# Performance work log

Hardware: AMD Instinct MI355X
Metric: run time of the kernel (lower is better)

Reference implementation:

```python
import jax, jax.numpy as jnp
import numpy as np

C_IN = 128
C_INNER = 128


def setup_inputs() -> dict:
    key = jax.random.key(0)
    ks = jax.random.split(key, 9)
    b, c, h, w = 4, C_IN, 64, 64
    s = 1.0 / np.sqrt(c)
    x = jax.random.normal(ks[0], (b, c, h, w), dtype=jnp.float32)
    Wq = jax.random.normal(ks[1], (C_INNER, C_IN), dtype=jnp.float32) * s
    bq = jnp.zeros((C_INNER,), dtype=jnp.float32)
    Wk = jax.random.normal(ks[2], (C_INNER, C_IN), dtype=jnp.float32) * s
    bk = jnp.zeros((C_INNER,), dtype=jnp.float32)
    Wv = jax.random.normal(ks[3], (C_INNER, C_IN), dtype=jnp.float32) * s
    bv = jnp.zeros((C_INNER,), dtype=jnp.float32)
    Wo = jax.random.normal(ks[4], (C_IN, C_INNER), dtype=jnp.float32) * (1.0 / np.sqrt(C_INNER))
    bo = jnp.zeros((C_IN,), dtype=jnp.float32)
    return {"x": x, "Wq": Wq, "bq": bq, "Wk": Wk, "bk": bk,
            "Wv": Wv, "bv": bv, "Wo": Wo, "bo": bo}


def _conv1x1(x, W, bias):
    # x: (b,c,h,w), W: (o,c) -> (b,o,h,w)
    return jnp.einsum('oc,bchw->bohw', W, x) + bias[None, :, None, None]


def reference(x, Wq, bq, Wk, bk, Wv, bv, Wo, bo):
    b, c, h, w = x.shape
    ci = Wq.shape[0]
    n = h * w
    q = _conv1x1(x, Wq, bq).reshape(b, ci, n)          # (b, ci, n)
    k = _conv1x1(x, Wk, bk).reshape(b, ci, n)          # (b, ci, n)
    v = _conv1x1(x, Wv, bv).reshape(b, ci, n)          # (b, ci, n)
    # attn = softmax(q^T @ k) over keys
    attn = jnp.einsum('bci,bcj->bij', q, k)            # (b, n, n)
    attn = jax.nn.softmax(attn, axis=-1)
    out = jnp.einsum('bij,bcj->bci', attn, v)          # (b, ci, n)
    out = out.reshape(b, ci, h, w)
    out = _conv1x1(out, Wo, bo)
    return out + x
```

## Files before the change

### kernel.cpp

```cpp
#include <hip/hip_runtime.h>
#include <math.h>
#include <stdint.h>

#define CDIM 128
#define NTOT 4096
#define LOG2E 1.44269504f

typedef _Float16 f16x8 __attribute__((ext_vector_type(8)));
typedef float floatx4 __attribute__((ext_vector_type(4)));

static __device__ __forceinline__ floatx4 mfma16(f16x8 a, f16x8 b, floatx4 c) {
    return __builtin_amdgcn_mfma_f32_16x16x32_f16(a, b, c, 0, 0, 0);
}
static __device__ __forceinline__ unsigned short f2h(float f) {
    _Float16 h = (_Float16)f;
    return __builtin_bit_cast(unsigned short, h);
}
static __device__ __forceinline__ float h2f(unsigned short u) {
    return (float)__builtin_bit_cast(_Float16, u);
}
static __device__ __forceinline__ float fexp2(float x) {
#if __has_builtin(__builtin_amdgcn_exp2f)
    return __builtin_amdgcn_exp2f(x);
#else
    return exp2f(x);
#endif
}

#define SWZ(row, cc) ((((row) << 7)) + ((((cc) ^ ((row) & 15))) << 3))
#define SWZ8(row, cc) ((((row) << 6)) + ((((cc) ^ ((row) & 7))) << 3))

static __device__ __forceinline__ void gload_lds16(const void* g, void* l) {
    __builtin_amdgcn_global_load_lds(
        (const __attribute__((address_space(1))) void*)g,
        (__attribute__((address_space(3))) void*)l, 16, 0, 0);
}

__global__ __launch_bounds__(256) void qkv_proj_kernel(
    const float* __restrict__ x,
    const float* __restrict__ Wq, const float* __restrict__ Wk,
    const float* __restrict__ Wv,
    const float* __restrict__ bq, const float* __restrict__ bk,
    const float* __restrict__ bv,
    unsigned short* __restrict__ qo, unsigned short* __restrict__ ko,
    unsigned short* __restrict__ vo)
{
    __shared__ __align__(16) unsigned short Xs[64][136];
    __shared__ __align__(16) unsigned short Ws[3][64][136];

    const int t = threadIdx.x, b = blockIdx.y, n0 = blockIdx.x * 64;
    const int zo = blockIdx.z * 64;
    const int w = t >> 6, quad = (t >> 4) & 3, l15 = t & 15;

    {
        const int n = (t & 15) * 4;
        const int c = (t >> 4) * 8;
        float4 xr[8];
        #pragma unroll
        for (int j = 0; j < 8; ++j)
            xr[j] = *(const float4*)&x[((size_t)b * CDIM + c + j) * NTOT + n0 + n];
        #pragma unroll
        for (int k = 0; k < 4; ++k) {
            ushort4 ulo, uhi;
            ulo.x = f2h(((const float*)&xr[0])[k]);
            ulo.y = f2h(((const float*)&xr[1])[k]);
            ulo.z = f2h(((const float*)&xr[2])[k]);
            ulo.w = f2h(((const float*)&xr[3])[k]);
            uhi.x = f2h(((const float*)&xr[4])[k]);
            uhi.y = f2h(((const float*)&xr[5])[k]);
            uhi.z = f2h(((const float*)&xr[6])[k]);
            uhi.w = f2h(((const float*)&xr[7])[k]);
            *(ushort4*)&Xs[n + k][c]     = ulo;
            *(ushort4*)&Xs[n + k][c + 4] = uhi;
        }
    }
    {
        const int o = t >> 2, ch = (t & 3) * 32;
        #pragma unroll
        for (int s = 0; s < 3; ++s) {
            const float* W = (s == 0) ? Wq : (s == 1) ? Wk : Wv;
            #pragma unroll
            for (int i = 0; i < 8; ++i) {
                float4 f4 = *(const float4*)&W[(size_t)(zo + o) * CDIM + ch + i * 4];
                ushort4 u = { f2h(f4.x), f2h(f4.y), f2h(f4.z), f2h(f4.w) };
                *(ushort4*)&Ws[s][o][ch + i * 4] = u;
            }
        }
    }
    __syncthreads();

    f16x8 xf[4];
    #pragma unroll
    for (int f = 0; f < 4; ++f)
        xf[f] = *(const f16x8*)&Xs[w * 16 + l15][f * 32 + quad * 8];

    #pragma unroll
    for (int s = 0; s < 2; ++s) {
        const float* bias = s ? bk : bq;
        unsigned short* dst = s ? ko : qo;
        const float sc = (s == 0) ? LOG2E : 1.0f;
        #pragma unroll
        for (int ot = 0; ot < 4; ++ot) {
            floatx4 acc = (floatx4){0.f, 0.f, 0.f, 0.f};
            #pragma unroll
            for (int f = 0; f < 4; ++f) {
                f16x8 aW = *(const f16x8*)&Ws[s][ot * 16 + l15][f * 32 + quad * 8];
                acc = mfma16(aW, xf[f], acc);
            }
            const int ob = zo + ot * 16 + quad * 4;
            ushort4 u;
            u.x = f2h((acc[0] + bias[ob + 0]) * sc);
            u.y = f2h((acc[1] + bias[ob + 1]) * sc);
            u.z = f2h((acc[2] + bias[ob + 2]) * sc);
            u.w = f2h((acc[3] + bias[ob + 3]) * sc);
            *(ushort4*)&dst[((size_t)b * NTOT + n0 + w * 16 + l15) * CDIM + ob] = u;
        }
    }
    #pragma unroll
    for (int ot = 0; ot < 4; ++ot) {
        floatx4 acc = (floatx4){0.f, 0.f, 0.f, 0.f};
        #pragma unroll
        for (int f = 0; f < 4; ++f) {
            f16x8 bW = *(const f16x8*)&Ws[2][ot * 16 + l15][f * 32 + quad * 8];
            acc = mfma16(xf[f], bW, acc);
        }
        const int o = zo + ot * 16 + l15;
        const float bv_ = bv[o];
        ushort4 u;
        u.x = f2h(acc[0] + bv_); u.y = f2h(acc[1] + bv_);
        u.z = f2h(acc[2] + bv_); u.w = f2h(acc[3] + bv_);
        *(ushort4*)&vo[((size_t)b * CDIM + o) * NTOT + n0 + w * 16 + quad * 4] = u;
    }
}

__global__ __launch_bounds__(512) void attn_kernel(
    const unsigned short* __restrict__ qg,
    const unsigned short* __restrict__ kg,
    const unsigned short* __restrict__ vg,
    unsigned short* __restrict__ Op,
    float* __restrict__ Ms, float* __restrict__ Ls)
{
    __shared__ __align__(16) unsigned short Kb[2][64 * 128];
    __shared__ __align__(16) unsigned short Vb[3][128 * 64];
    __shared__ __align__(16) unsigned short Ps[256 * 64];

    const int t = threadIdx.x;
    const int w = t >> 6, quad = (t >> 4) & 3, l15 = t & 15;

    const int bid = blockIdx.x;
    const int swz = ((bid & 7) << 5) | (bid >> 3);
    const int gidx = swz >> 4;
    const int b = gidx & 3;
    const int z = gidx >> 2;
    const int i0 = (swz & 15) * 256;
    const int jbase = z * 1024;
    const size_t vbase = (size_t)b * CDIM * NTOT;

    f16x8 bQ[2][4];
    #pragma unroll
    for (int nt = 0; nt < 2; ++nt) {
        const size_t qrow = ((size_t)b * NTOT + i0 + w * 32 + nt * 16 + l15) * CDIM;
        #pragma unroll
        for (int f = 0; f < 4; ++f)
            bQ[nt][f] = *(const f16x8*)&qg[qrow + f * 32 + quad * 8];
    }

    auto stageK = [&](unsigned short* Kd, int j0) {
        const size_t kbase = ((size_t)b * NTOT + j0) * CDIM;
        #pragma unroll
        for (int r = 0; r < 2; ++r) {
            const int flat = r * 512 + t;
            const int ldsoff = (r * 512 + (t & ~63)) * 8;
            const int krow = flat >> 4, kcc = flat & 15;
            gload_lds16(&kg[kbase + (size_t)krow * CDIM + ((kcc ^ (krow & 15)) << 3)],
                        &Kd[ldsoff]);
        }
    };
    auto stageV = [&](unsigned short* Vd, int j0) {
        const size_t vrow0 = vbase + j0;
        #pragma unroll
        for (int r = 0; r < 2; ++r) {
            const int flat = r * 512 + t;
            const int ldsoff = (r * 512 + (t & ~63)) * 8;
            const int vrow = flat >> 3, vcc = flat & 7;
            gload_lds16(&vg[vrow0 + (size_t)vrow * NTOT + ((vcc ^ (vrow & 7)) << 3)],
                        &Vd[ldsoff]);
        }
    };

    floatx4 accO[2][8];
    #pragma unroll
    for (int nt = 0; nt < 2; ++nt)
        #pragma unroll
        for (int dt = 0; dt < 8; ++dt) accO[nt][dt] = (floatx4){0.f, 0.f, 0.f, 0.f};
    float m_run[2] = {-INFINITY, -INFINITY};
    float l_part[2] = {0.f, 0.f};

    floatx4 accT[2][4];
    uint2 pu[2][4];
    f16x8 bP[2][2];

    auto QK = [&](const unsigned short* Kd) {
        #pragma unroll
        for (int nt = 0; nt < 2; ++nt)
            #pragma unroll
            for (int jt = 0; jt < 4; ++jt) accT[nt][jt] = (floatx4){0.f, 0.f, 0.f, 0.f};
        __builtin_amdgcn_s_setprio(1);
        #pragma unroll
        for (int jt = 0; jt < 4; ++jt)
            #pragma unroll
            for (int f = 0; f < 4; ++f) {
                f16x8 aK = *(const f16x8*)&Kd[SWZ(jt * 16 + l15, f * 4 + quad)];
                accT[0][jt] = mfma16(aK, bQ[0][f], accT[0][jt]);
                accT[1][jt] = mfma16(aK, bQ[1][f], accT[1][jt]);
            }
        __builtin_amdgcn_s_setprio(0);
    };
    auto RB = [&]() {
        #pragma unroll
        for (int nt = 0; nt < 2; ++nt) {
            const int prow = w * 32 + nt * 16 + l15;
            #pragma unroll
            for (int kb = 0; kb < 2; ++kb)
                bP[nt][kb] = *(const f16x8*)&Ps[SWZ8(prow, kb * 4 + quad)];
        }
    };
    auto PV = [&](const unsigned short* Vd) {
        __builtin_amdgcn_s_setprio(1);
        #pragma unroll
        for (int dt = 0; dt < 8; ++dt)
            #pragma unroll
            for (int kb = 0; kb < 2; ++kb) {
                f16x8 aV = *(const f16x8*)&Vd[SWZ8(dt * 16 + l15, kb * 4 + quad)];
                accO[0][dt] = mfma16(aV, bP[0][kb], accO[0][dt]);
                accO[1][dt] = mfma16(aV, bP[1][kb], accO[1][dt]);
            }
        __builtin_amdgcn_s_setprio(0);
    };
    auto SM = [&]() {
        #pragma unroll
        for (int nt = 0; nt < 2; ++nt) {
            float tm = accT[nt][0][0];
            #pragma unroll
            for (int jt = 0; jt < 4; ++jt)
                #pragma unroll
                for (int r = 0; r < 4; ++r) tm = fmaxf(tm, accT[nt][jt][r]);
            tm = fmaxf(tm, __shfl_xor(tm, 16));
            tm = fmaxf(tm, __shfl_xor(tm, 32));
            if (__ballot(tm > m_run[nt] + 11.5416f)) {
                const float m_new = fmaxf(m_run[nt], tm);
                const float alpha = fexp2(m_run[nt] - m_new);
                m_run[nt] = m_new;
                l_part[nt] *= alpha;
                #pragma unroll
                for (int dt = 0; dt < 8; ++dt) {
                    accO[nt][dt][0] *= alpha; accO[nt][dt][1] *= alpha;
                    accO[nt][dt][2] *= alpha; accO[nt][dt][3] *= alpha;
                }
            }
            const float mcur = m_run[nt];
            float ps = 0.f;
            #pragma unroll
            for (int jt = 0; jt < 4; ++jt) {
                float p0 = fexp2(accT[nt][jt][0] - mcur);
                float p1 = fexp2(accT[nt][jt][1] - mcur);
                float p2 = fexp2(accT[nt][jt][2] - mcur);
                float p3 = fexp2(accT[nt][jt][3] - mcur);
                ps += (p0 + p1) + (p2 + p3);
                pu[nt][jt].x = __builtin_bit_cast(unsigned int,
                                   __builtin_amdgcn_cvt_pkrtz(p0, p1));
                pu[nt][jt].y = __builtin_bit_cast(unsigned int,
                                   __builtin_amdgcn_cvt_pkrtz(p2, p3));
            }
            l_part[nt] += ps;
        }
    };
    auto WP = [&]() {
        #pragma unroll
        for (int nt = 0; nt < 2; ++nt) {
            const int prow = w * 32 + nt * 16 + l15;
            #pragma unroll
            for (int jt = 0; jt < 4; ++jt)
                *(uint2*)&Ps[SWZ8(prow, 2 * jt + (quad >> 1)) + (quad & 1) * 4] =
                    pu[nt][jt];
        }
    };

    stageK(Kb[0], jbase);
    stageV(Vb[0], jbase);
    unsigned short *Kc = Kb[0], *Kn = Kb[1];
    unsigned short *Vprev = Vb[0], *Vcur = Vb[1], *Vnext = Vb[2];

    asm volatile("s_waitcnt vmcnt(0) lgkmcnt(0)" ::: "memory");
    __builtin_amdgcn_s_barrier();
    stageK(Kn, jbase + 64);
    stageV(Vcur, jbase + 64);
    QK(Kc);
    SM();
    WP();
    { unsigned short* tp = Kc; Kc = Kn; Kn = tp; }

    for (int it = 1; it <= 14; ++it) {
        asm volatile("s_waitcnt vmcnt(2) lgkmcnt(0)" ::: "memory");
        __builtin_amdgcn_s_barrier();
        RB();
        stageK(Kn, jbase + (it + 1) * 64);
        stageV(Vnext, jbase + (it + 1) * 64);
        QK(Kc);
        PV(Vprev);
        SM();
        WP();
        { unsigned short* tp = Kc; Kc = Kn; Kn = tp; }
        { unsigned short* tv = Vprev; Vprev = Vcur; Vcur = Vnext; Vnext = tv; }
    }

    asm volatile("s_waitcnt vmcnt(2) lgkmcnt(0)" ::: "memory");
    __builtin_amdgcn_s_barrier();
    RB();
    QK(Kc);
    PV(Vprev);
    SM();
    WP();
    Vprev = Vcur;
    asm volatile("s_waitcnt vmcnt(0) lgkmcnt(0)" ::: "memory");
    __builtin_amdgcn_s_barrier();
    RB();
    PV(Vprev);

    #pragma unroll
    for (int nt = 0; nt < 2; ++nt) {
        float lf = l_part[nt];
        lf += __shfl_xor(lf, 16);
        lf += __shfl_xor(lf, 32);
        const float inv = 1.0f / lf;
        const size_t orow =
            (((size_t)z * 4 + b) * NTOT + i0 + w * 32 + nt * 16 + l15) * CDIM;
        #pragma unroll
        for (int dt = 0; dt < 8; ++dt) {
            ushort4 u;
            u.x = f2h(accO[nt][dt][0] * inv); u.y = f2h(accO[nt][dt][1] * inv);
            u.z = f2h(accO[nt][dt][2] * inv); u.w = f2h(accO[nt][dt][3] * inv);
            *(ushort4*)&Op[orow + dt * 16 + quad * 4] = u;
        }
        if (quad == 0) {
            const int idx = (z * 4 + b) * NTOT + i0 + w * 32 + nt * 16 + l15;
            Ms[idx] = m_run[nt];
            Ls[idx] = lf;
        }
    }
}

__global__ __launch_bounds__(256) void out_proj_kernel(
    const unsigned short* __restrict__ Op,
    const float* __restrict__ Ms, const float* __restrict__ Ls,
    const float* __restrict__ Wo, const float* __restrict__ bo,
    const float* __restrict__ x, float* __restrict__ out)
{
    __shared__ __align__(16) unsigned short As[64][136];
    __shared__ __align__(16) unsigned short Ws[64][136];

    const int t = threadIdx.x, b = blockIdx.y, n0 = blockIdx.x * 64;
    const int zo = blockIdx.z * 64;
    const int w = t >> 6, quad = (t >> 4) & 3, l15 = t & 15;

    const size_t PER = (size_t)NTOT * 4 * CDIM;

    #pragma unroll
    for (int r = 0; r < 4; ++r) {
        int flat = r * 256 + t;
        int row = flat >> 4, c16 = (flat & 15) * 8;
        const int bn = b * NTOT + n0 + row;
        float m0 = Ms[bn], m1 = Ms[bn + 16384], m2 = Ms[bn + 32768], m3 = Ms[bn + 49152];
        float M = fmaxf(fmaxf(m0, m1), fmaxf(m2, m3));
        float w0 = Ls[bn]         * fexp2(m0 - M);
        float w1 = Ls[bn + 16384] * fexp2(m1 - M);
        float w2 = Ls[bn + 32768] * fexp2(m2 - M);
        float w3 = Ls[bn + 49152] * fexp2(m3 - M);
        const float inv = 1.0f / (w0 + w1 + w2 + w3);
        w0 *= inv; w1 *= inv; w2 *= inv; w3 *= inv;

        const size_t base = (size_t)bn * CDIM + c16;
        uint4 a0 = *(const uint4*)&Op[base];
        uint4 a1 = *(const uint4*)&Op[PER + base];
        uint4 a2 = *(const uint4*)&Op[2 * PER + base];
        uint4 a3 = *(const uint4*)&Op[3 * PER + base];
        const unsigned short* p0 = (const unsigned short*)&a0;
        const unsigned short* p1 = (const unsigned short*)&a1;
        const unsigned short* p2 = (const unsigned short*)&a2;
        const unsigned short* p3 = (const unsigned short*)&a3;
        unsigned short mv[8];
        #pragma unroll
        for (int j = 0; j < 8; ++j)
            mv[j] = f2h(w0 * h2f(p0[j]) + w1 * h2f(p1[j]) +
                        w2 * h2f(p2[j]) + w3 * h2f(p3[j]));
        *(uint4*)&As[row][c16] = *(const uint4*)mv;
    }
    {
        int o = t >> 2, ch = (t & 3) * 32;
        #pragma unroll
        for (int i = 0; i < 8; ++i) {
            float4 f4 = *(const float4*)&Wo[(size_t)(zo + o) * CDIM + ch + i * 4];
            ushort4 u = { f2h(f4.x), f2h(f4.y), f2h(f4.z), f2h(f4.w) };
            *(ushort4*)&Ws[o][ch + i * 4] = u;
        }
    }
    __syncthreads();

    f16x8 bA[4];
    #pragma unroll
    for (int f = 0; f < 4; ++f)
        bA[f] = *(const f16x8*)&As[w * 16 + l15][f * 32 + quad * 8];

    #pragma unroll
    for (int ot = 0; ot < 4; ++ot) {
        floatx4 acc = (floatx4){0.f, 0.f, 0.f, 0.f};
        #pragma unroll
        for (int f = 0; f < 4; ++f) {
            f16x8 aW = *(const f16x8*)&Ws[ot * 16 + l15][f * 32 + quad * 8];
            acc = mfma16(aW, bA[f], acc);
        }
        const int ob = zo + ot * 16 + quad * 4;
        #pragma unroll
        for (int r = 0; r < 4; ++r) {
            size_t idx = ((size_t)b * CDIM + ob + r) * NTOT + n0 + w * 16 + l15;
            out[idx] = acc[r] + bo[ob + r] + x[idx];
        }
    }
}

extern "C" void kernel_launch(void* const* d_in, const int* in_sizes, int n_in,
                              void* d_out, int out_size, void* d_ws, size_t ws_size,
                              hipStream_t stream)
{
    const float* x  = (const float*)d_in[0];
    const float* Wq = (const float*)d_in[1];
    const float* bq = (const float*)d_in[2];
    const float* Wk = (const float*)d_in[3];
    const float* bk = (const float*)d_in[4];
    const float* Wv = (const float*)d_in[5];
    const float* bv = (const float*)d_in[6];
    const float* Wo = (const float*)d_in[7];
    const float* bo = (const float*)d_in[8];
    float* out = (float*)d_out;

    const size_t PER = (size_t)4 * CDIM * NTOT;
    unsigned short* q_ws  = (unsigned short*)d_ws;
    unsigned short* k_ws  = q_ws + PER;
    unsigned short* v_ws  = k_ws + PER;
    unsigned short* op_ws = v_ws + PER;
    float*          ms_ws = (float*)(op_ws + 4 * PER);
    float*          ls_ws = ms_ws + 4 * 16384;

    qkv_proj_kernel<<<dim3(64, 4, 2), dim3(256), 0, stream>>>(
        x, Wq, Wk, Wv, bq, bk, bv, q_ws, k_ws, v_ws);
    attn_kernel<<<dim3(256), dim3(512), 0, stream>>>(
        q_ws, k_ws, v_ws, op_ws, ms_ws, ls_ws);
    out_proj_kernel<<<dim3(64, 4, 2), dim3(256), 0, stream>>>(
        op_ws, ms_ws, ls_ws, Wo, bo, x, out);
}
```

Baseline: 138.0 us.

## Feed P from registers to 16x16x16 MFMA and split keys eight ways

```diff
diff --git a/kernel.cpp b/kernel.cpp
--- a/kernel.cpp
+++ b/kernel.cpp
@@ -5,12 +5,17 @@
 #define CDIM 128
 #define NTOT 4096
 #define LOG2E 1.44269504f
+#define NZ 8
 
 typedef _Float16 f16x8 __attribute__((ext_vector_type(8)));
+typedef _Float16 f16x4 __attribute__((ext_vector_type(4)));
 typedef float floatx4 __attribute__((ext_vector_type(4)));
 
 static __device__ __forceinline__ floatx4 mfma16(f16x8 a, f16x8 b, floatx4 c) {
     return __builtin_amdgcn_mfma_f32_16x16x32_f16(a, b, c, 0, 0, 0);
+}
+static __device__ __forceinline__ floatx4 mfma16k16(f16x4 a, f16x4 b, floatx4 c) {
+    return __builtin_amdgcn_mfma_f32_16x16x16f16(a, b, c, 0, 0, 0);
 }
 static __device__ __forceinline__ unsigned short f2h(float f) {
     _Float16 h = (_Float16)f;
@@ -142,18 +147,17 @@
 {
     __shared__ __align__(16) unsigned short Kb[2][64 * 128];
     __shared__ __align__(16) unsigned short Vb[3][128 * 64];
-    __shared__ __align__(16) unsigned short Ps[256 * 64];
 
     const int t = threadIdx.x;
     const int w = t >> 6, quad = (t >> 4) & 3, l15 = t & 15;
 
     const int bid = blockIdx.x;
-    const int swz = ((bid & 7) << 5) | (bid >> 3);
+    const int swz = ((bid & 7) << 6) | (bid >> 3);
     const int gidx = swz >> 4;
     const int b = gidx & 3;
     const int z = gidx >> 2;
     const int i0 = (swz & 15) * 256;
-    const int jbase = z * 1024;
+    const int jbase = z * (NTOT / NZ);
     const size_t vbase = (size_t)b * CDIM * NTOT;
 
     f16x8 bQ[2][4];
@@ -198,7 +202,6 @@
 
     floatx4 accT[2][4];
     uint2 pu[2][4];
-    f16x8 bP[2][2];
 
     auto QK = [&](const unsigned short* Kd) {
         #pragma unroll
@@ -216,24 +219,18 @@
             }
         __builtin_amdgcn_s_setprio(0);
     };
-    auto RB = [&]() {
-        #pragma unroll
-        for (int nt = 0; nt < 2; ++nt) {
-            const int prow = w * 32 + nt * 16 + l15;
-            #pragma unroll
-            for (int kb = 0; kb < 2; ++kb)
-                bP[nt][kb] = *(const f16x8*)&Ps[SWZ8(prow, kb * 4 + quad)];
-        }
-    };
     auto PV = [&](const unsigned short* Vd) {
         __builtin_amdgcn_s_setprio(1);
         #pragma unroll
         for (int dt = 0; dt < 8; ++dt)
             #pragma unroll
-            for (int kb = 0; kb < 2; ++kb) {
-                f16x8 aV = *(const f16x8*)&Vd[SWZ8(dt * 16 + l15, kb * 4 + quad)];
-                accO[0][dt] = mfma16(aV, bP[0][kb], accO[0][dt]);
-                accO[1][dt] = mfma16(aV, bP[1][kb], accO[1][dt]);
+            for (int jt = 0; jt < 4; ++jt) {
+                f16x4 aV = *(const f16x4*)
+                    &Vd[SWZ8(dt * 16 + l15, 2 * jt + (quad >> 1)) + (quad & 1) * 4];
+                accO[0][dt] = mfma16k16(aV, __builtin_bit_cast(f16x4, pu[0][jt]),
+                                        accO[0][dt]);
+                accO[1][dt] = mfma16k16(aV, __builtin_bit_cast(f16x4, pu[1][jt]),
+                                        accO[1][dt]);
             }
         __builtin_amdgcn_s_setprio(0);
     };
@@ -275,16 +272,6 @@
             l_part[nt] += ps;
         }
     };
-    auto WP = [&]() {
-        #pragma unroll
-        for (int nt = 0; nt < 2; ++nt) {
-            const int prow = w * 32 + nt * 16 + l15;
-            #pragma unroll
-            for (int jt = 0; jt < 4; ++jt)
-                *(uint2*)&Ps[SWZ8(prow, 2 * jt + (quad >> 1)) + (quad & 1) * 4] =
-                    pu[nt][jt];
-        }
-    };
 
     stageK(Kb[0], jbase);
     stageV(Vb[0], jbase);
@@ -297,35 +284,28 @@
     stageV(Vcur, jbase + 64);
     QK(Kc);
     SM();
-    WP();
     { unsigned short* tp = Kc; Kc = Kn; Kn = tp; }
 
-    for (int it = 1; it <= 14; ++it) {
+    for (int it = 1; it <= 6; ++it) {
         asm volatile("s_waitcnt vmcnt(2) lgkmcnt(0)" ::: "memory");
         __builtin_amdgcn_s_barrier();
-        RB();
         stageK(Kn, jbase + (it + 1) * 64);
         stageV(Vnext, jbase + (it + 1) * 64);
         QK(Kc);
         PV(Vprev);
         SM();
-        WP();
         { unsigned short* tp = Kc; Kc = Kn; Kn = tp; }
         { unsigned short* tv = Vprev; Vprev = Vcur; Vcur = Vnext; Vnext = tv; }
     }
 
     asm volatile("s_waitcnt vmcnt(2) lgkmcnt(0)" ::: "memory");
     __builtin_amdgcn_s_barrier();
-    RB();
     QK(Kc);
     PV(Vprev);
     SM();
-    WP();
-    Vprev = Vcur;
     asm volatile("s_waitcnt vmcnt(0) lgkmcnt(0)" ::: "memory");
     __builtin_amdgcn_s_barrier();
-    RB();
-    PV(Vprev);
+    PV(Vcur);
 
     #pragma unroll
     for (int nt = 0; nt < 2; ++nt) {
@@ -370,29 +350,31 @@
         int flat = r * 256 + t;
         int row = flat >> 4, c16 = (flat & 15) * 8;
         const int bn = b * NTOT + n0 + row;
-        float m0 = Ms[bn], m1 = Ms[bn + 16384], m2 = Ms[bn + 32768], m3 = Ms[bn + 49152];
-        float M = fmaxf(fmaxf(m0, m1), fmaxf(m2, m3));
-        float w0 = Ls[bn]         * fexp2(m0 - M);
-        float w1 = Ls[bn + 16384] * fexp2(m1 - M);
-        float w2 = Ls[bn + 32768] * fexp2(m2 - M);
-        float w3 = Ls[bn + 49152] * fexp2(m3 - M);
-        const float inv = 1.0f / (w0 + w1 + w2 + w3);
-        w0 *= inv; w1 *= inv; w2 *= inv; w3 *= inv;
+
+        float m[NZ], lw[NZ];
+        float M = -INFINITY;
+        #pragma unroll
+        for (int zz = 0; zz < NZ; ++zz) { m[zz] = Ms[bn + zz * 16384]; M = fmaxf(M, m[zz]); }
+        float wsum = 0.f;
+        #pragma unroll
+        for (int zz = 0; zz < NZ; ++zz) {
+            lw[zz] = Ls[bn + zz * 16384] * fexp2(m[zz] - M);
+            wsum += lw[zz];
+        }
+        const float inv = 1.0f / wsum;
 
         const size_t base = (size_t)bn * CDIM + c16;
-        uint4 a0 = *(const uint4*)&Op[base];
-        uint4 a1 = *(const uint4*)&Op[PER + base];
-        uint4 a2 = *(const uint4*)&Op[2 * PER + base];
-        uint4 a3 = *(const uint4*)&Op[3 * PER + base];
-        const unsigned short* p0 = (const unsigned short*)&a0;
-        const unsigned short* p1 = (const unsigned short*)&a1;
-        const unsigned short* p2 = (const unsigned short*)&a2;
-        const unsigned short* p3 = (const unsigned short*)&a3;
+        float acc[8] = {0.f, 0.f, 0.f, 0.f, 0.f, 0.f, 0.f, 0.f};
+        #pragma unroll
+        for (int zz = 0; zz < NZ; ++zz) {
+            uint4 a = *(const uint4*)&Op[zz * PER + base];
+            const unsigned short* p = (const unsigned short*)&a;
+            #pragma unroll
+            for (int j = 0; j < 8; ++j) acc[j] += lw[zz] * h2f(p[j]);
+        }
         unsigned short mv[8];
         #pragma unroll
-        for (int j = 0; j < 8; ++j)
-            mv[j] = f2h(w0 * h2f(p0[j]) + w1 * h2f(p1[j]) +
-                        w2 * h2f(p2[j]) + w3 * h2f(p3[j]));
+        for (int j = 0; j < 8; ++j) mv[j] = f2h(acc[j] * inv);
         *(uint4*)&As[row][c16] = *(const uint4*)mv;
     }
     {
@@ -448,12 +430,12 @@
     unsigned short* k_ws  = q_ws + PER;
     unsigned short* v_ws  = k_ws + PER;
     unsigned short* op_ws = v_ws + PER;
-    float*          ms_ws = (float*)(op_ws + 4 * PER);
-    float*          ls_ws = ms_ws + 4 * 16384;
+    float*          ms_ws = (float*)(op_ws + (size_t)NZ * PER);
+    float*          ls_ws = ms_ws + (size_t)NZ * 16384;
 
     qkv_proj_kernel<<<dim3(64, 4, 2), dim3(256), 0, stream>>>(
         x, Wq, Wk, Wv, bq, bk, bv, q_ws, k_ws, v_ws);
-    attn_kernel<<<dim3(256), dim3(512), 0, stream>>>(
+    attn_kernel<<<dim3(512), dim3(512), 0, stream>>>(
         q_ws, k_ws, v_ws, op_ws, ms_ws, ls_ws);
     out_proj_kernel<<<dim3(64, 4, 2), dim3(256), 0, stream>>>(
         op_ws, ms_ws, ls_ws, Wo, bo, x, out);
```

New measurement: 153.9 us. 11.5% more time.

## Interleave softmax exponentials and rescaling with PV MFMAs in attention loop

Applied to the files above, without the earlier changes.

```diff
diff --git a/kernel.cpp b/kernel.cpp
--- a/kernel.cpp
+++ b/kernel.cpp
@@ -199,6 +199,7 @@
     floatx4 accT[2][4];
     uint2 pu[2][4];
     f16x8 bP[2][2];
+    float alpha[2], mcur[2], ps[2];
 
     auto QK = [&](const unsigned short* Kd) {
         #pragma unroll
@@ -225,8 +226,52 @@
                 bP[nt][kb] = *(const f16x8*)&Ps[SWZ8(prow, kb * 4 + quad)];
         }
     };
-    auto PV = [&](const unsigned short* Vd) {
-        __builtin_amdgcn_s_setprio(1);
+    auto SMpre = [&]() {
+        ps[0] = 0.f; ps[1] = 0.f;
+        #pragma unroll
+        for (int nt = 0; nt < 2; ++nt) {
+            float tm = accT[nt][0][0];
+            #pragma unroll
+            for (int jt = 0; jt < 4; ++jt)
+                #pragma unroll
+                for (int r = 0; r < 4; ++r) tm = fmaxf(tm, accT[nt][jt][r]);
+            tm = fmaxf(tm, __shfl_xor(tm, 16));
+            tm = fmaxf(tm, __shfl_xor(tm, 32));
+            const float mnew = fmaxf(m_run[nt], tm);
+            alpha[nt] = fexp2(m_run[nt] - mnew);
+            m_run[nt] = mnew;
+            mcur[nt] = mnew;
+            l_part[nt] *= alpha[nt];
+        }
+    };
+    auto SLICE = [&](int snt, int sjt) {
+        float p0 = fexp2(accT[snt][sjt][0] - mcur[snt]);
+        float p1 = fexp2(accT[snt][sjt][1] - mcur[snt]);
+        float p2 = fexp2(accT[snt][sjt][2] - mcur[snt]);
+        float p3 = fexp2(accT[snt][sjt][3] - mcur[snt]);
+        ps[snt] += (p0 + p1) + (p2 + p3);
+        pu[snt][sjt].x = __builtin_bit_cast(unsigned int,
+                             __builtin_amdgcn_cvt_pkrtz(p0, p1));
+        pu[snt][sjt].y = __builtin_bit_cast(unsigned int,
+                             __builtin_amdgcn_cvt_pkrtz(p2, p3));
+    };
+    auto PVSM = [&](const unsigned short* Vd) {
+        #pragma unroll
+        for (int dt = 0; dt < 8; ++dt) {
+            f16x8 aV0 = *(const f16x8*)&Vd[SWZ8(dt * 16 + l15, 0 * 4 + quad)];
+            f16x8 aV1 = *(const f16x8*)&Vd[SWZ8(dt * 16 + l15, 1 * 4 + quad)];
+            accO[0][dt] = mfma16(aV0, bP[0][0], accO[0][dt]);
+            accO[1][dt] = mfma16(aV0, bP[1][0], accO[1][dt]);
+            accO[0][dt] = mfma16(aV1, bP[0][1], accO[0][dt]);
+            accO[1][dt] = mfma16(aV1, bP[1][1], accO[1][dt]);
+            accO[0][dt][0] *= alpha[0]; accO[0][dt][1] *= alpha[0];
+            accO[0][dt][2] *= alpha[0]; accO[0][dt][3] *= alpha[0];
+            accO[1][dt][0] *= alpha[1]; accO[1][dt][1] *= alpha[1];
+            accO[1][dt][2] *= alpha[1]; accO[1][dt][3] *= alpha[1];
+            SLICE(dt >> 2, dt & 3);
+        }
+    };
+    auto PVonly = [&](const unsigned short* Vd) {
         #pragma unroll
         for (int dt = 0; dt < 8; ++dt)
             #pragma unroll
@@ -235,45 +280,6 @@
                 accO[0][dt] = mfma16(aV, bP[0][kb], accO[0][dt]);
                 accO[1][dt] = mfma16(aV, bP[1][kb], accO[1][dt]);
             }
-        __builtin_amdgcn_s_setprio(0);
-    };
-    auto SM = [&]() {
-        #pragma unroll
-        for (int nt = 0; nt < 2; ++nt) {
-            float tm = accT[nt][0][0];
-            #pragma unroll
-            for (int jt = 0; jt < 4; ++jt)
-                #pragma unroll
-                for (int r = 0; r < 4; ++r) tm = fmaxf(tm, accT[nt][jt][r]);
-            tm = fmaxf(tm, __shfl_xor(tm, 16));
-            tm = fmaxf(tm, __shfl_xor(tm, 32));
-            if (__ballot(tm > m_run[nt] + 11.5416f)) {
-                const float m_new = fmaxf(m_run[nt], tm);
-                const float alpha = fexp2(m_run[nt] - m_new);
-                m_run[nt] = m_new;
-                l_part[nt] *= alpha;
-                #pragma unroll
-                for (int dt = 0; dt < 8; ++dt) {
-                    accO[nt][dt][0] *= alpha; accO[nt][dt][1] *= alpha;
-                    accO[nt][dt][2] *= alpha; accO[nt][dt][3] *= alpha;
-                }
-            }
-            const float mcur = m_run[nt];
-            float ps = 0.f;
-            #pragma unroll
-            for (int jt = 0; jt < 4; ++jt) {
-                float p0 = fexp2(accT[nt][jt][0] - mcur);
-                float p1 = fexp2(accT[nt][jt][1] - mcur);
-                float p2 = fexp2(accT[nt][jt][2] - mcur);
-                float p3 = fexp2(accT[nt][jt][3] - mcur);
-                ps += (p0 + p1) + (p2 + p3);
-                pu[nt][jt].x = __builtin_bit_cast(unsigned int,
-                                   __builtin_amdgcn_cvt_pkrtz(p0, p1));
-                pu[nt][jt].y = __builtin_bit_cast(unsigned int,
-                                   __builtin_amdgcn_cvt_pkrtz(p2, p3));
-            }
-            l_part[nt] += ps;
-        }
     };
     auto WP = [&]() {
         #pragma unroll
@@ -296,7 +302,10 @@
     stageK(Kn, jbase + 64);
     stageV(Vcur, jbase + 64);
     QK(Kc);
-    SM();
+    SMpre();
+    #pragma unroll
+    for (int s = 0; s < 8; ++s) SLICE(s >> 2, s & 3);
+    l_part[0] += ps[0]; l_part[1] += ps[1];
     WP();
     { unsigned short* tp = Kc; Kc = Kn; Kn = tp; }
 
@@ -307,8 +316,9 @@
         stageK(Kn, jbase + (it + 1) * 64);
         stageV(Vnext, jbase + (it + 1) * 64);
         QK(Kc);
-        PV(Vprev);
-        SM();
+        SMpre();
+        PVSM(Vprev);
+        l_part[0] += ps[0]; l_part[1] += ps[1];
         WP();
         { unsigned short* tp = Kc; Kc = Kn; Kn = tp; }
         { unsigned short* tv = Vprev; Vprev = Vcur; Vcur = Vnext; Vnext = tv; }
@@ -318,14 +328,15 @@
     __builtin_amdgcn_s_barrier();
     RB();
     QK(Kc);
-    PV(Vprev);
-    SM();
+    SMpre();
+    PVSM(Vprev);
+    l_part[0] += ps[0]; l_part[1] += ps[1];
     WP();
     Vprev = Vcur;
     asm volatile("s_waitcnt vmcnt(0) lgkmcnt(0)" ::: "memory");
     __builtin_amdgcn_s_barrier();
     RB();
-    PV(Vprev);
+    PVonly(Vprev);
 
     #pragma unroll
     for (int nt = 0; nt < 2; ++nt) {
```

Measured after the change: 136.3 us. No clear change (-1.2%).
